# Optimization experiments

Hardware: AMD Instinct MI355X
Metric: run time of the kernel (lower is better)

The kernel has to match this reference:

```python
import jax, jax.numpy as jnp
import numpy as np

B, S, D, H = 2, 2048, 1024, 16
HD = D // H
DI = int(8 / 3 * D)  # 2730
EPS = 1e-5


def rmsnorm(x, gamma):
    rms = jnp.sqrt(jnp.mean(x * x, axis=-1, keepdims=True) + EPS)
    return (x / rms) * gamma


def rope(x):
    # x: [B, H, S, HD]; rotate interleaved even/odd pairs, concat halves
    hd = x.shape[-1]
    seq = x.shape[2]
    theta = 1.0 / (10000.0 ** (jnp.arange(0, hd, 2, dtype=jnp.float32) / hd))  # [HD/2]
    ang = jnp.arange(seq, dtype=jnp.float32)[:, None] * theta  # [S, HD/2]
    cos = jnp.cos(ang)[None, None]  # [1,1,S,HD/2]
    sin = jnp.sin(ang)[None, None]
    x1, x2 = x[..., ::2], x[..., 1::2]
    return jnp.concatenate([x1 * cos - x2 * sin, x1 * sin + x2 * cos], axis=-1)


def setup_inputs() -> dict:
    key = jax.random.key(0)
    ks = jax.random.split(key, 8)
    w = lambda k, shape: (jax.random.normal(k, shape, jnp.float32) * 0.02)
    return {
        "x": jax.random.normal(ks[0], (B, S, D), jnp.float32),
        "mask": jnp.tril(jnp.ones((1, 1, S, S), jnp.int32)),  # causal
        "gamma_attn": jnp.ones((D,), jnp.float32),
        "w_qkv": w(ks[1], (3 * D, D)),
        "b_qkv": jnp.zeros((3 * D,), jnp.float32),
        "w_out": w(ks[2], (D, D)),
        "b_out": jnp.zeros((D,), jnp.float32),
        "gamma_ffn": jnp.ones((D,), jnp.float32),
        "w1": w(ks[3], (DI, D)),
        "b1": jnp.zeros((DI,), jnp.float32),
        "w2": w(ks[4], (DI, D)),
        "b2": jnp.zeros((DI,), jnp.float32),
        "w3": w(ks[5], (D, DI)),
        "b3": jnp.zeros((D,), jnp.float32),
    }


def reference(x, mask, gamma_attn, w_qkv, b_qkv, w_out, b_out,
              gamma_ffn, w1, b1, w2, b2, w3, b3):
    batch, seq, d_model = x.shape
    # --- attn norm (pre-norm; residual uses normalized x, matching source) ---
    xn = rmsnorm(x, gamma_attn)
    # --- MHA ---
    qkv = xn @ w_qkv.T + b_qkv  # [B,S,3D]
    q, k, v = jnp.split(qkv, 3, axis=-1)
    q = q.reshape(batch, seq, H, HD).transpose(0, 2, 1, 3)  # [B,H,S,HD]
    k = k.reshape(batch, seq, H, HD).transpose(0, 2, 1, 3)
    v = v.reshape(batch, seq, H, HD).transpose(0, 2, 1, 3)
    q = rope(q)
    k = rope(k)
    scores = jnp.einsum("bhqd,bhkd->bhqk", q, k) / jnp.sqrt(jnp.float32(HD))
    scores = jnp.where(mask == 0, jnp.float32(-jnp.inf), scores)
    attn = jax.nn.softmax(scores, axis=-1)
    out = jnp.einsum("bhqk,bhkd->bhqd", attn, v)
    out = out.transpose(0, 2, 1, 3).reshape(batch, seq, d_model)
    attn_out = out @ w_out.T + b_out
    h = xn + attn_out
    # --- FFN norm + SwiGLU ---
    hn = rmsnorm(h, gamma_ffn)
    gate = jax.nn.silu(hn @ w2.T + b2)
    ff = (hn @ w1.T + b1) * gate
    ffn_out = ff @ w3.T + b3
    return hn + ffn_out
```

## Files before the change

### kernel.cpp

```cpp
#include <hip/hip_runtime.h>

typedef unsigned short u16;
typedef unsigned int u32;
typedef __attribute__((ext_vector_type(8))) short short8;
typedef __attribute__((ext_vector_type(4))) float f32x4;

#define Bt 2
#define St 2048
#define Dm 1024
#define Ht 16
#define HD 64
#define DI 2730
#define DIP 2816
#define DIP2 5632
#define Mrows 4096

typedef const __attribute__((address_space(1))) unsigned char* gp_t;
typedef __attribute__((address_space(3))) unsigned char* lp_t;
#define GLDS16(g, l) __builtin_amdgcn_global_load_lds((gp_t)(g), (lp_t)(l), 16, 0, 0)

__device__ __forceinline__ float bf2f(u16 b){
  union { float f; u32 i; } v; v.i = ((u32)b) << 16; return v.f;
}
__device__ __forceinline__ u16 f2bf(float f){
  union { float f; u32 i; } v; v.f = f;
  u32 u = v.i;
  return (u16)((u + 0x7FFFu + ((u >> 16) & 1u)) >> 16);
}
__device__ __forceinline__ uint2 pack4(float a, float b, float c, float d){
  uint2 o;
  o.x = (u32)f2bf(a) | ((u32)f2bf(b) << 16);
  o.y = (u32)f2bf(c) | ((u32)f2bf(d) << 16);
  return o;
}

__global__ __launch_bounds__(256) void prep_k(const float* __restrict__ w_qkv,
                                              const float* __restrict__ w_out,
                                              const float* __restrict__ w1,
                                              const float* __restrict__ w2,
                                              const float* __restrict__ w3,
                                              const float* __restrict__ b1,
                                              const float* __restrict__ b2,
                                              const float* __restrict__ x,
                                              const float* __restrict__ gamma,
                                              u16* __restrict__ w_qkvb,
                                              u16* __restrict__ w_outb,
                                              u16* __restrict__ w12i,
                                              u16* __restrict__ w3b,
                                              float* __restrict__ b12i,
                                              u16* __restrict__ xn)
{
  __shared__ float red[4];
  int bidx = blockIdx.x;
  const int t = threadIdx.x;
  if (bidx < 3072){
    const int i4 = (bidx * 256 + t) * 4;
    float4 v = *(const float4*)(w_qkv + i4);
    *(uint2*)(w_qkvb + i4) = pack4(v.x, v.y, v.z, v.w);
    return;
  }
  bidx -= 3072;
  if (bidx < 1024){
    const int i4 = (bidx * 256 + t) * 4;
    float4 v = *(const float4*)(w_out + i4);
    *(uint2*)(w_outb + i4) = pack4(v.x, v.y, v.z, v.w);
    return;
  }
  bidx -= 1024;
  if (bidx < 2816){
    const int i4 = (bidx * 256 + t) * 4;
    const int k = i4 >> 10, c = i4 & 1023;
    uint2 o = {0, 0};
    if (k < DI){
      float4 v = *(const float4*)(w1 + i4);
      o = pack4(v.x, v.y, v.z, v.w);
    }
    *(uint2*)(w12i + ((size_t)(2 * k)) * 1024 + c) = o;
    return;
  }
  bidx -= 2816;
  if (bidx < 2816){
    const int i4 = (bidx * 256 + t) * 4;
    const int k = i4 >> 10, c = i4 & 1023;
    uint2 o = {0, 0};
    if (k < DI){
      float4 v = *(const float4*)(w2 + i4);
      o = pack4(v.x, v.y, v.z, v.w);
    }
    *(uint2*)(w12i + ((size_t)(2 * k + 1)) * 1024 + c) = o;
    return;
  }
  bidx -= 2816;
  if (bidx < 2816){
    const int i4 = (bidx * 256 + t) * 4;
    const int n = i4 / DIP, kk = i4 % DIP;
    float e[4];
    #pragma unroll
    for (int j = 0; j < 4; ++j)
      e[j] = (kk + j < DI) ? w3[(size_t)n * DI + kk + j] : 0.0f;
    *(uint2*)(w3b + i4) = pack4(e[0], e[1], e[2], e[3]);
    return;
  }
  bidx -= 2816;
  if (bidx < 6){
    const int i0 = (bidx * 256 + t) * 4;
    #pragma unroll
    for (int j = 0; j < 4; ++j){
      const int idx = i0 + j;
      if (idx < DIP2){
        const int k = idx >> 1;
        b12i[idx] = (k < DI) ? ((idx & 1) ? b2[k] : b1[k]) : 0.0f;
      }
    }
    return;
  }
  bidx -= 6;
  {
    const size_t base = (size_t)bidx * Dm + t * 4;
    float4 v = *(const float4*)(x + base);
    float ss = v.x*v.x + v.y*v.y + v.z*v.z + v.w*v.w;
    #pragma unroll
    for (int sh = 1; sh < 64; sh <<= 1) ss += __shfl_xor(ss, sh, 64);
    if ((t & 63) == 0) red[t >> 6] = ss;
    __syncthreads();
    float tot = red[0] + red[1] + red[2] + red[3];
    float rinv = 1.0f / sqrtf(tot * (1.0f / 1024.0f) + 1e-5f);
    float4 gv = *(const float4*)(gamma + t * 4);
    *(uint2*)(xn + base) = pack4(v.x * rinv * gv.x, v.y * rinv * gv.y,
                                 v.z * rinv * gv.z, v.w * rinv * gv.w);
  }
}

__global__ __launch_bounds__(256) void rmsnorm2_k(const u16* xa,
                                                  const u16* __restrict__ xb,
                                                  const float* __restrict__ g,
                                                  u16* o)
{
  __shared__ float red[4];
  const int row = blockIdx.x, t = threadIdx.x;
  const size_t base = (size_t)row * Dm + t * 4;
  uint2 va = *(const uint2*)(xa + base);
  uint2 vb = *(const uint2*)(xb + base);
  float f0 = bf2f((u16)(va.x & 0xffff)) + bf2f((u16)(vb.x & 0xffff));
  float f1 = bf2f((u16)(va.x >> 16))    + bf2f((u16)(vb.x >> 16));
  float f2 = bf2f((u16)(va.y & 0xffff)) + bf2f((u16)(vb.y & 0xffff));
  float f3 = bf2f((u16)(va.y >> 16))    + bf2f((u16)(vb.y >> 16));
  float ss = f0*f0 + f1*f1 + f2*f2 + f3*f3;
  #pragma unroll
  for (int sh = 1; sh < 64; sh <<= 1) ss += __shfl_xor(ss, sh, 64);
  if ((t & 63) == 0) red[t >> 6] = ss;
  __syncthreads();
  float tot = red[0] + red[1] + red[2] + red[3];
  float rinv = 1.0f / sqrtf(tot * (1.0f / 1024.0f) + 1e-5f);
  float4 gv = *(const float4*)(g + t * 4);
  uint2 outp;
  outp.x = (u32)f2bf(f0 * rinv * gv.x) | ((u32)f2bf(f1 * rinv * gv.y) << 16);
  outp.y = (u32)f2bf(f2 * rinv * gv.z) | ((u32)f2bf(f3 * rinv * gv.w) << 16);
  *(uint2*)(o + base) = outp;
}

#define BK 32
template<int RES, int WF>
__global__ __launch_bounds__(256) void gemm_bt(const u16* __restrict__ A,
                                               const u16* __restrict__ Bw,
                                               const float* __restrict__ bias,
                                               const u16* __restrict__ res,
                                               void* __restrict__ Cv,
                                               int N, int K, int lda, int ldc)
{
  __shared__ __align__(16) u16 lA[128 * BK];
  __shared__ __align__(16) u16 lB[128 * BK];
  const int tid = threadIdx.x;
  const int m0 = blockIdx.x * 128;
  const int n0 = blockIdx.y * 128;
  const int wave = tid >> 6, lane = tid & 63;
  const int wm = (wave >> 1) * 64, wn = (wave & 1) * 64;
  const int lm = lane & 15, lq = lane >> 4;

  f32x4 acc[4][4] = {};
  const int rl = lane >> 2, seg = lane & 3;

  const int nk = K / BK;
  for (int kt = 0; kt < nk; ++kt){
    const int k0 = kt * BK;
    __syncthreads();
    #pragma unroll
    for (int i = 0; i < 2; ++i){
      const int ra = wave * 32 + i * 16 + rl;
      const int kc = seg ^ ((ra >> 1) & 3);
      GLDS16(A  + (size_t)(m0 + ra) * lda + k0 + kc * 8, &lA[(wave * 32 + i * 16) * BK]);
      GLDS16(Bw + (size_t)(n0 + ra) * K   + k0 + kc * 8, &lB[(wave * 32 + i * 16) * BK]);
    }
    __syncthreads();
    short8 af[4], bfr[4];
    #pragma unroll
    for (int i = 0; i < 4; ++i){
      int r = wm + i * 16 + lm;
      af[i] = *(const short8*)&lA[r * BK + ((lq ^ ((r >> 1) & 3)) * 8)];
    }
    #pragma unroll
    for (int j = 0; j < 4; ++j){
      int r = wn + j * 16 + lm;
      bfr[j] = *(const short8*)&lB[r * BK + ((lq ^ ((r >> 1) & 3)) * 8)];
    }
    #pragma unroll
    for (int i = 0; i < 4; ++i)
      #pragma unroll
      for (int j = 0; j < 4; ++j)
        acc[i][j] = __builtin_amdgcn_mfma_f32_16x16x32_bf16(af[i], bfr[j], acc[i][j], 0, 0, 0);
  }

  #pragma unroll
  for (int i = 0; i < 4; ++i){
    const int row = m0 + wm + i * 16 + lq * 4;
    #pragma unroll
    for (int j = 0; j < 4; ++j){
      const int col = n0 + wn + j * 16 + lm;
      const float bb = bias[col];
      #pragma unroll
      for (int r = 0; r < 4; ++r){
        float v = acc[i][j][r] + bb;
        if (RES) v += bf2f(res[(size_t)(row + r) * ldc + col]);
        if (WF) ((float*)Cv)[(size_t)(row + r) * ldc + col] = v;
        else    ((u16*)Cv)[(size_t)(row + r) * ldc + col] = f2bf(v);
      }
    }
  }
}

__global__ __launch_bounds__(256) void gemm_ffn(const u16* __restrict__ A,
                                                const u16* __restrict__ Bw,
                                                const float* __restrict__ bias,
                                                u16* __restrict__ ff)
{
  __shared__ __align__(16) u16 lA[128 * BK];
  __shared__ __align__(16) u16 lB[128 * BK];
  const int tid = threadIdx.x;
  const int m0 = blockIdx.x * 128;
  const int n0 = blockIdx.y * 128;
  const int wave = tid >> 6, lane = tid & 63;
  const int wm = (wave >> 1) * 64, wn = (wave & 1) * 64;
  const int lm = lane & 15, lq = lane >> 4;

  f32x4 acc[4][4] = {};
  const int rl = lane >> 2, seg = lane & 3;

  for (int kt = 0; kt < 1024 / BK; ++kt){
    const int k0 = kt * BK;
    __syncthreads();
    #pragma unroll
    for (int i = 0; i < 2; ++i){
      const int ra = wave * 32 + i * 16 + rl;
      const int kc = seg ^ ((ra >> 1) & 3);
      GLDS16(A  + (size_t)(m0 + ra) * 1024 + k0 + kc * 8, &lA[(wave * 32 + i * 16) * BK]);
      GLDS16(Bw + (size_t)(n0 + ra) * 1024 + k0 + kc * 8, &lB[(wave * 32 + i * 16) * BK]);
    }
    __syncthreads();
    short8 af[4], bfr[4];
    #pragma unroll
    for (int i = 0; i < 4; ++i){
      int r = wm + i * 16 + lm;
      af[i] = *(const short8*)&lA[r * BK + ((lq ^ ((r >> 1) & 3)) * 8)];
    }
    #pragma unroll
    for (int j = 0; j < 4; ++j){
      int r = wn + j * 16 + lm;
      bfr[j] = *(const short8*)&lB[r * BK + ((lq ^ ((r >> 1) & 3)) * 8)];
    }
    #pragma unroll
    for (int i = 0; i < 4; ++i)
      #pragma unroll
      for (int j = 0; j < 4; ++j)
        acc[i][j] = __builtin_amdgcn_mfma_f32_16x16x32_bf16(af[i], bfr[j], acc[i][j], 0, 0, 0);
  }

  #pragma unroll
  for (int i = 0; i < 4; ++i){
    const int row = m0 + wm + i * 16 + lq * 4;
    #pragma unroll
    for (int j = 0; j < 4; ++j){
      const int col = n0 + wn + j * 16 + lm;
      const float bb = bias[col];
      const int kcol = col >> 1;
      #pragma unroll
      for (int r = 0; r < 4; ++r){
        float v = acc[i][j][r] + bb;
        float g = __shfl_xor(v, 1, 64);
        if ((lm & 1) == 0){
          float ffv = v * (g / (1.0f + __expf(-g)));
          ff[(size_t)(row + r) * DIP + kcol] = f2bf(ffv);
        }
      }
    }
  }
}

template<int RES, int WF>
__global__ __launch_bounds__(256) void gemm_bt64(const u16* __restrict__ A,
                                                 const u16* __restrict__ Bw,
                                                 const float* __restrict__ bias,
                                                 const u16* __restrict__ res,
                                                 void* __restrict__ Cv,
                                                 int N, int K, int lda, int ldc)
{
  __shared__ __align__(16) u16 lA[128 * BK];
  __shared__ __align__(16) u16 lB[64 * BK];
  const int tid = threadIdx.x;
  const int m0 = blockIdx.x * 128;
  const int n0 = blockIdx.y * 64;
  const int wave = tid >> 6, lane = tid & 63;
  const int wm = wave * 32;
  const int lm = lane & 15, lq = lane >> 4;

  f32x4 acc[2][4] = {};
  const int rl = lane >> 2, seg = lane & 3;

  const int nk = K / BK;
  for (int kt = 0; kt < nk; ++kt){
    const int k0 = kt * BK;
    __syncthreads();
    #pragma unroll
    for (int i = 0; i < 2; ++i){
      const int ra = wave * 32 + i * 16 + rl;
      const int kc = seg ^ ((ra >> 1) & 3);
      GLDS16(A + (size_t)(m0 + ra) * lda + k0 + kc * 8, &lA[(wave * 32 + i * 16) * BK]);
    }
    {
      const int rb = wave * 16 + rl;
      const int kc = seg ^ ((rb >> 1) & 3);
      GLDS16(Bw + (size_t)(n0 + rb) * K + k0 + kc * 8, &lB[(wave * 16) * BK]);
    }
    __syncthreads();
    short8 af[2], bfr[4];
    #pragma unroll
    for (int i = 0; i < 2; ++i){
      int r = wm + i * 16 + lm;
      af[i] = *(const short8*)&lA[r * BK + ((lq ^ ((r >> 1) & 3)) * 8)];
    }
    #pragma unroll
    for (int j = 0; j < 4; ++j){
      int r = j * 16 + lm;
      bfr[j] = *(const short8*)&lB[r * BK + ((lq ^ ((r >> 1) & 3)) * 8)];
    }
    #pragma unroll
    for (int i = 0; i < 2; ++i)
      #pragma unroll
      for (int j = 0; j < 4; ++j)
        acc[i][j] = __builtin_amdgcn_mfma_f32_16x16x32_bf16(af[i], bfr[j], acc[i][j], 0, 0, 0);
  }

  #pragma unroll
  for (int i = 0; i < 2; ++i){
    const int row = m0 + wm + i * 16 + lq * 4;
    #pragma unroll
    for (int j = 0; j < 4; ++j){
      const int col = n0 + j * 16 + lm;
      const float bb = bias[col];
      #pragma unroll
      for (int r = 0; r < 4; ++r){
        float v = acc[i][j][r] + bb;
        if (RES) v += bf2f(res[(size_t)(row + r) * ldc + col]);
        if (WF) ((float*)Cv)[(size_t)(row + r) * ldc + col] = v;
        else    ((u16*)Cv)[(size_t)(row + r) * ldc + col] = f2bf(v);
      }
    }
  }
}

__global__ __launch_bounds__(256) void rv_k(const u16* __restrict__ qkv,
                                            u16* __restrict__ qr,
                                            u16* __restrict__ kr,
                                            u16* __restrict__ vT)
{
  __shared__ u16 tbuf[64][66];
  const int bid = blockIdx.x;
  const int tid = threadIdx.x;
  if (bid < 16384){
    const int g = bid * 4 + (tid >> 6);
    const int d = tid & 63;
    const int h = g & 15, m = g >> 4;
    const int s = m & (St - 1), b = m >> 11;
    const int p = d & 31, hi = d >> 5;
    const float theta = __expf(-(float)p * 0.28782313662425575f);
    const float ang = (float)s * theta;
    const float c = cosf(ang), sn = sinf(ang);
    const u16* base = qkv + (size_t)m * 3072;
    float x1q = bf2f(base[h * 64 + 2 * p]);
    float x2q = bf2f(base[h * 64 + 2 * p + 1]);
    float x1k = bf2f(base[1024 + h * 64 + 2 * p]);
    float x2k = bf2f(base[1024 + h * 64 + 2 * p + 1]);
    float vq = (hi == 0) ? (x1q * c - x2q * sn) : (x1q * sn + x2q * c);
    float vk = (hi == 0) ? (x1k * c - x2k * sn) : (x1k * sn + x2k * c);
    const size_t oidx = ((size_t)(b * 16 + h) * St + s) * 64 + d;
    qr[oidx] = f2bf(vq * 0.125f);
    kr[oidx] = f2bf(vk);
  } else {
    const int vt = bid - 16384;
    const int st = vt & 31, bh = vt >> 5;
    const int b = bh >> 4, h = bh & 15;
    const int c2 = (tid & 31) * 2, rg = tid >> 5;
    #pragma unroll
    for (int it = 0; it < 8; ++it){
      int row = rg + it * 8;
      u32 v = *(const u32*)&qkv[(size_t)(b * St + st * 64 + row) * 3072 + 2048 + h * 64 + c2];
      *(u32*)&tbuf[row][c2] = v;
    }
    __syncthreads();
    const int sl = tid & 63;
    #pragma unroll
    for (int it = 0; it < 16; ++it){
      int d = (tid >> 6) + it * 4;
      vT[((size_t)bh * 64 + d) * St + st * 64 + sl] = tbuf[sl][d];
    }
  }
}

__global__ __launch_bounds__(256) void fattn_k(const u16* __restrict__ qr,
                                               const u16* __restrict__ kr,
                                               const u16* __restrict__ vT,
                                               u16* __restrict__ ctx)
{
  __shared__ __align__(16) u16 lK[64 * 80];
  __shared__ __align__(16) u16 lV[64 * 80];
  __shared__ __align__(16) u16 pP[4][16 * 72];

  const int bid = blockIdx.x;
  const int bh = bid & 31;
  const int jj = 15 - (bid >> 5);
  const int qt0 = jj << 7;
  const int tid = threadIdx.x;
  const int wave = tid >> 6, lane = tid & 63;
  const int lm = lane & 15, lq = lane >> 4;

  const u16* Kb = kr + (size_t)bh * St * 64;
  const u16* Vb = vT + (size_t)bh * 64 * St;
  const u16* Qb = qr + ((size_t)bh * St + qt0 + wave * 32) * 64;

  short8 qf[2][2];
  #pragma unroll
  for (int st = 0; st < 2; ++st){
    qf[st][0] = *(const short8*)&Qb[(st * 16 + lm) * 64 + lq * 8];
    qf[st][1] = *(const short8*)&Qb[(st * 16 + lm) * 64 + 32 + lq * 8];
  }

  f32x4 o[2][4] = {};
  float ls[2][4] = {};
  const int kend = qt0 + 128;

  for (int kb = 0; kb < kend; kb += 64){
    __syncthreads();
    #pragma unroll
    for (int p = 0; p < 2; ++p){
      const int idx = p * 256 + tid;
      const int r0 = idx >> 3, sg = idx & 7;
      uint4 kv = *(const uint4*)(Kb + (size_t)(kb + r0) * 64 + sg * 8);
      uint4 vv = *(const uint4*)(Vb + (size_t)r0 * St + kb + sg * 8);
      *(uint4*)&lK[r0 * 80 + sg * 8] = kv;
      *(uint4*)&lV[r0 * 80 + sg * 8] = vv;
    }
    __syncthreads();
    f32x4 sc[2][4];
    #pragma unroll
    for (int nt = 0; nt < 4; ++nt){
      const u16* Krow = &lK[(nt * 16 + lm) * 80];
      short8 kf0 = *(const short8*)&Krow[lq * 8];
      short8 kf1 = *(const short8*)&Krow[32 + lq * 8];
      #pragma unroll
      for (int st = 0; st < 2; ++st){
        f32x4 a = {};
        a = __builtin_amdgcn_mfma_f32_16x16x32_bf16(qf[st][0], kf0, a, 0, 0, 0);
        a = __builtin_amdgcn_mfma_f32_16x16x32_bf16(qf[st][1], kf1, a, 0, 0, 0);
        sc[st][nt] = a;
      }
    }
    #pragma unroll
    for (int st = 0; st < 2; ++st){
      const int minrow = qt0 + wave * 32 + st * 16;
      if (kb + 63 > minrow){
        const int rowb = minrow + lq * 4;
        #pragma unroll
        for (int nt = 0; nt < 4; ++nt){
          const int key = kb + nt * 16 + lm;
          #pragma unroll
          for (int r = 0; r < 4; ++r)
            if (key > rowb + r) sc[st][nt][r] = -1e30f;
        }
      }
    }
    short8 pf[2][2];
    #pragma unroll
    for (int st = 0; st < 2; ++st){
      #pragma unroll
      for (int nt = 0; nt < 4; ++nt)
        #pragma unroll
        for (int r = 0; r < 4; ++r){
          float p = __expf(sc[st][nt][r] - 12.0f);
          ls[st][r] += p;
          pP[wave][(lq * 4 + r) * 72 + nt * 16 + lm] = f2bf(p);
        }
      pf[st][0] = *(const short8*)&pP[wave][lm * 72 + lq * 8];
      pf[st][1] = *(const short8*)&pP[wave][lm * 72 + 32 + lq * 8];
    }
    #pragma unroll
    for (int ct = 0; ct < 4; ++ct){
      const u16* Vrow = &lV[(ct * 16 + lm) * 80];
      short8 vf0 = *(const short8*)&Vrow[lq * 8];
      short8 vf1 = *(const short8*)&Vrow[32 + lq * 8];
      #pragma unroll
      for (int st = 0; st < 2; ++st){
        o[st][ct] = __builtin_amdgcn_mfma_f32_16x16x32_bf16(pf[st][0], vf0, o[st][ct], 0, 0, 0);
        o[st][ct] = __builtin_amdgcn_mfma_f32_16x16x32_bf16(pf[st][1], vf1, o[st][ct], 0, 0, 0);
      }
    }
  }
  #pragma unroll
  for (int sh = 1; sh < 16; sh <<= 1)
    #pragma unroll
    for (int st = 0; st < 2; ++st)
      #pragma unroll
      for (int r = 0; r < 4; ++r)
        ls[st][r] += __shfl_xor(ls[st][r], sh, 64);
  const int b = bh >> 4, h = bh & 15;
  #pragma unroll
  for (int st = 0; st < 2; ++st)
    #pragma unroll
    for (int r = 0; r < 4; ++r){
      const int s = qt0 + wave * 32 + st * 16 + lq * 4 + r;
      const float inv = 1.0f / ls[st][r];
      #pragma unroll
      for (int ct = 0; ct < 4; ++ct){
        const int d = ct * 16 + lm;
        ctx[((size_t)(b * St + s)) * Dm + h * 64 + d] = f2bf(o[st][ct][r] * inv);
      }
    }
}

extern "C" void kernel_launch(void* const* d_in, const int* in_sizes, int n_in,
                              void* d_out, int out_size, void* d_ws, size_t ws_size,
                              hipStream_t stream) {
  (void)in_sizes; (void)n_in; (void)out_size; (void)ws_size;
  const float* x          = (const float*)d_in[0];
  const float* gamma_attn = (const float*)d_in[2];
  const float* w_qkv      = (const float*)d_in[3];
  const float* b_qkv      = (const float*)d_in[4];
  const float* w_out      = (const float*)d_in[5];
  const float* b_out      = (const float*)d_in[6];
  const float* gamma_ffn  = (const float*)d_in[7];
  const float* w1         = (const float*)d_in[8];
  const float* b1         = (const float*)d_in[9];
  const float* w2         = (const float*)d_in[10];
  const float* b2         = (const float*)d_in[11];
  const float* w3         = (const float*)d_in[12];
  const float* b3         = (const float*)d_in[13];
  float* out = (float*)d_out;
  char* ws = (char*)d_ws;

  u16* w_qkvb  = (u16*)(ws + 0);
  u16* w_outb  = (u16*)(ws + 6291456);
  u16* w12i    = (u16*)(ws + 8388608);
  u16* w3b     = (u16*)(ws + 19922944);
  float* b12i  = (float*)(ws + 25690112);
  u16* xn      = (u16*)(ws + 25712640);
  u16* hn      = xn;
  u16* qkv     = (u16*)(ws + 34101248);
  u16* ctx     = (u16*)(ws + 34101248);
  u16* att     = (u16*)(ws + 42489856);
  u16* ff      = (u16*)(ws + 34101248);
  u16* qr      = (u16*)(ws + 59267072);
  u16* kr      = (u16*)(ws + 67655680);
  u16* vT      = (u16*)(ws + 76044288);

  dim3 blk(256);
  prep_k<<<16646, blk, 0, stream>>>(w_qkv, w_out, w1, w2, w3, b1, b2, x, gamma_attn,
                                    w_qkvb, w_outb, w12i, w3b, b12i, xn);
  gemm_bt<0,0><<<dim3(32, 24), blk, 0, stream>>>(xn, w_qkvb, b_qkv, nullptr, qkv, 3072, 1024, 1024, 3072);
  rv_k<<<17408, blk, 0, stream>>>(qkv, qr, kr, vT);
  fattn_k<<<512, blk, 0, stream>>>(qr, kr, vT, ctx);
  gemm_bt64<0,0><<<dim3(32, 16), blk, 0, stream>>>(ctx, w_outb, b_out, nullptr, att, 1024, 1024, 1024, 1024);
  rmsnorm2_k<<<Mrows, blk, 0, stream>>>(xn, att, gamma_ffn, hn);
  gemm_ffn<<<dim3(32, 44), blk, 0, stream>>>(hn, w12i, b12i, ff);
  gemm_bt64<1,1><<<dim3(32, 16), blk, 0, stream>>>(ff, w3b, b3, hn, out, 1024, DIP, DIP, 1024);
}
```

Measured before the change: 386.5 us.

## Fuse RoPE, Q scaling and V transpose into the QKV GEMM epilogue

Replaces the generic QKV GEMM plus separate rv_k kernel with a specialised gemm_qkv. Its epilogue applies RoPE (using a lane shuffle to fetch the paired element) and the Q scale, and writes Q/K directly in head-major layout. V is transposed through shared memory and written to vT. This removes the round trip of the 24 MB qkv intermediate and one kernel launch, at the cost of cos/sin work in the epilogue and scattered 2-byte stores for Q/K. It also adds an occupancy hint of 4 blocks per SM to gemm_ffn.

Result: slower. 834.9 us (+116.0%).

```diff
diff --git a/kernel.cpp b/kernel.cpp
--- a/kernel.cpp
+++ b/kernel.cpp
@@ -160,16 +160,16 @@
 }
 
 #define BK 32
-template<int RES, int WF>
-__global__ __launch_bounds__(256) void gemm_bt(const u16* __restrict__ A,
-                                               const u16* __restrict__ Bw,
-                                               const float* __restrict__ bias,
-                                               const u16* __restrict__ res,
-                                               void* __restrict__ Cv,
-                                               int N, int K, int lda, int ldc)
+__global__ __launch_bounds__(256) void gemm_qkv(const u16* __restrict__ A,
+                                                const u16* __restrict__ Bw,
+                                                const float* __restrict__ bias,
+                                                u16* __restrict__ qr,
+                                                u16* __restrict__ kr,
+                                                u16* __restrict__ vT)
 {
-  __shared__ __align__(16) u16 lA[128 * BK];
-  __shared__ __align__(16) u16 lB[128 * BK];
+  __shared__ __align__(16) u16 smem[8704];
+  u16* lA = smem;
+  u16* lB = smem + 4096;
   const int tid = threadIdx.x;
   const int m0 = blockIdx.x * 128;
   const int n0 = blockIdx.y * 128;
@@ -180,16 +180,15 @@
   f32x4 acc[4][4] = {};
   const int rl = lane >> 2, seg = lane & 3;
 
-  const int nk = K / BK;
-  for (int kt = 0; kt < nk; ++kt){
+  for (int kt = 0; kt < 1024 / BK; ++kt){
     const int k0 = kt * BK;
     __syncthreads();
     #pragma unroll
     for (int i = 0; i < 2; ++i){
       const int ra = wave * 32 + i * 16 + rl;
       const int kc = seg ^ ((ra >> 1) & 3);
-      GLDS16(A  + (size_t)(m0 + ra) * lda + k0 + kc * 8, &lA[(wave * 32 + i * 16) * BK]);
-      GLDS16(Bw + (size_t)(n0 + ra) * K   + k0 + kc * 8, &lB[(wave * 32 + i * 16) * BK]);
+      GLDS16(A  + (size_t)(m0 + ra) * 1024 + k0 + kc * 8, &lA[(wave * 32 + i * 16) * BK]);
+      GLDS16(Bw + (size_t)(n0 + ra) * 1024 + k0 + kc * 8, &lB[(wave * 32 + i * 16) * BK]);
     }
     __syncthreads();
     short8 af[4], bfr[4];
@@ -210,28 +209,72 @@
         acc[i][j] = __builtin_amdgcn_mfma_f32_16x16x32_bf16(af[i], bfr[j], acc[i][j], 0, 0, 0);
   }
 
-  #pragma unroll
-  for (int i = 0; i < 4; ++i){
-    const int row = m0 + wm + i * 16 + lq * 4;
-    #pragma unroll
-    for (int j = 0; j < 4; ++j){
-      const int col = n0 + wn + j * 16 + lm;
-      const float bb = bias[col];
-      #pragma unroll
-      for (int r = 0; r < 4; ++r){
-        float v = acc[i][j][r] + bb;
-        if (RES) v += bf2f(res[(size_t)(row + r) * ldc + col]);
-        if (WF) ((float*)Cv)[(size_t)(row + r) * ldc + col] = v;
-        else    ((u16*)Cv)[(size_t)(row + r) * ldc + col] = f2bf(v);
-      }
-    }
-  }
-}
-
-__global__ __launch_bounds__(256) void gemm_ffn(const u16* __restrict__ A,
-                                                const u16* __restrict__ Bw,
-                                                const float* __restrict__ bias,
-                                                u16* __restrict__ ff)
+  if (blockIdx.y < 16){
+    const int isq = (blockIdx.y < 8);
+    const int partbase = isq ? 0 : 1024;
+    u16* dst = isq ? qr : kr;
+    const float qs = isq ? 0.125f : 1.0f;
+    #pragma unroll
+    for (int i = 0; i < 4; ++i){
+      const int row = m0 + wm + i * 16 + lq * 4;
+      #pragma unroll
+      for (int j = 0; j < 4; ++j){
+        const int col = n0 + wn + j * 16 + lm;
+        const int cl = col - partbase;
+        const int h = cl >> 6, d = cl & 63;
+        const int p = d >> 1;
+        const float theta = __expf(-(float)p * 0.28782313662425575f);
+        const float bb = bias[col];
+        const int dp = (lm & 1) ? (32 + p) : p;
+        #pragma unroll
+        for (int r = 0; r < 4; ++r){
+          const int s = row + r;
+          const int sl = s & (St - 1), b = s >> 11;
+          float v = acc[i][j][r] + bb;
+          float pt = __shfl_xor(v, 1, 64);
+          float ang = (float)sl * theta;
+          float c = cosf(ang), sn = sinf(ang);
+          float outv = ((lm & 1) == 0) ? (v * c - pt * sn) : (pt * sn + v * c);
+          dst[((size_t)(b * 16 + h) * St + sl) * 64 + dp] = f2bf(outv * qs);
+        }
+      }
+    }
+  } else {
+    const int hbase = (n0 - 2048) >> 6;
+    const int b = m0 >> 11;
+    const int sl0 = m0 & (St - 1);
+    u16 (*tv)[136] = (u16(*)[136])smem;
+    for (int hh = 0; hh < 2; ++hh){
+      __syncthreads();
+      if ((wn >> 6) == hh){
+        #pragma unroll
+        for (int i = 0; i < 4; ++i){
+          const int rloc = wm + i * 16 + lq * 4;
+          #pragma unroll
+          for (int j = 0; j < 4; ++j){
+            const int dcol = j * 16 + lm;
+            const float bb = bias[n0 + wn + j * 16 + lm];
+            #pragma unroll
+            for (int r = 0; r < 4; ++r)
+              tv[dcol][rloc + r] = f2bf(acc[i][j][r] + bb);
+          }
+        }
+      }
+      __syncthreads();
+      const int d = tid >> 2, sgm = tid & 3;
+      u16* dstv = vT + ((size_t)((b * 16 + hbase + hh) * 64 + d)) * St + sl0 + sgm * 32;
+      const u16* src = &tv[d][sgm * 32];
+      #pragma unroll
+      for (int w = 0; w < 4; ++w)
+        *(uint4*)(dstv + w * 8) = *(const uint4*)(src + w * 8);
+    }
+  }
+}
+
+__global__ __launch_bounds__(256, 4) void gemm_ffn(const u16* __restrict__ A,
+                                                   const u16* __restrict__ Bw,
+                                                   const float* __restrict__ bias,
+                                                   u16* __restrict__ ff)
 {
   __shared__ __align__(16) u16 lA[128 * BK];
   __shared__ __align__(16) u16 lB[128 * BK];
@@ -363,54 +406,6 @@
         if (WF) ((float*)Cv)[(size_t)(row + r) * ldc + col] = v;
         else    ((u16*)Cv)[(size_t)(row + r) * ldc + col] = f2bf(v);
       }
-    }
-  }
-}
-
-__global__ __launch_bounds__(256) void rv_k(const u16* __restrict__ qkv,
-                                            u16* __restrict__ qr,
-                                            u16* __restrict__ kr,
-                                            u16* __restrict__ vT)
-{
-  __shared__ u16 tbuf[64][66];
-  const int bid = blockIdx.x;
-  const int tid = threadIdx.x;
-  if (bid < 16384){
-    const int g = bid * 4 + (tid >> 6);
-    const int d = tid & 63;
-    const int h = g & 15, m = g >> 4;
-    const int s = m & (St - 1), b = m >> 11;
-    const int p = d & 31, hi = d >> 5;
-    const float theta = __expf(-(float)p * 0.28782313662425575f);
-    const float ang = (float)s * theta;
-    const float c = cosf(ang), sn = sinf(ang);
-    const u16* base = qkv + (size_t)m * 3072;
-    float x1q = bf2f(base[h * 64 + 2 * p]);
-    float x2q = bf2f(base[h * 64 + 2 * p + 1]);
-    float x1k = bf2f(base[1024 + h * 64 + 2 * p]);
-    float x2k = bf2f(base[1024 + h * 64 + 2 * p + 1]);
-    float vq = (hi == 0) ? (x1q * c - x2q * sn) : (x1q * sn + x2q * c);
-    float vk = (hi == 0) ? (x1k * c - x2k * sn) : (x1k * sn + x2k * c);
-    const size_t oidx = ((size_t)(b * 16 + h) * St + s) * 64 + d;
-    qr[oidx] = f2bf(vq * 0.125f);
-    kr[oidx] = f2bf(vk);
-  } else {
-    const int vt = bid - 16384;
-    const int st = vt & 31, bh = vt >> 5;
-    const int b = bh >> 4, h = bh & 15;
-    const int c2 = (tid & 31) * 2, rg = tid >> 5;
-    #pragma unroll
-    for (int it = 0; it < 8; ++it){
-      int row = rg + it * 8;
-      u32 v = *(const u32*)&qkv[(size_t)(b * St + st * 64 + row) * 3072 + 2048 + h * 64 + c2];
-      *(u32*)&tbuf[row][c2] = v;
-    }
-    __syncthreads();
-    const int sl = tid & 63;
-    #pragma unroll
-    for (int it = 0; it < 16; ++it){
-      int d = (tid >> 6) + it * 4;
-      vT[((size_t)bh * 64 + d) * St + st * 64 + sl] = tbuf[sl][d];
     }
   }
 }
@@ -562,7 +557,6 @@
   float* b12i  = (float*)(ws + 25690112);
   u16* xn      = (u16*)(ws + 25712640);
   u16* hn      = xn;
-  u16* qkv     = (u16*)(ws + 34101248);
   u16* ctx     = (u16*)(ws + 34101248);
   u16* att     = (u16*)(ws + 42489856);
   u16* ff      = (u16*)(ws + 34101248);
@@ -573,8 +567,7 @@
   dim3 blk(256);
   prep_k<<<16646, blk, 0, stream>>>(w_qkv, w_out, w1, w2, w3, b1, b2, x, gamma_attn,
                                     w_qkvb, w_outb, w12i, w3b, b12i, xn);
-  gemm_bt<0,0><<<dim3(32, 24), blk, 0, stream>>>(xn, w_qkvb, b_qkv, nullptr, qkv, 3072, 1024, 1024, 3072);
-  rv_k<<<17408, blk, 0, stream>>>(qkv, qr, kr, vT);
+  gemm_qkv<<<dim3(32, 24), blk, 0, stream>>>(xn, w_qkvb, b_qkv, qr, kr, vT);
   fattn_k<<<512, blk, 0, stream>>>(qr, kr, vT, ctx);
   gemm_bt64<0,0><<<dim3(32, 16), blk, 0, stream>>>(ctx, w_outb, b_out, nullptr, att, 1024, 1024, 1024, 1024);
   rmsnorm2_k<<<Mrows, blk, 0, stream>>>(xn, att, gamma_ffn, hn);
```
